# Performance work log

Measured on AMD Instinct MI355X. Metric: run time of the kernel, lower is better.

The kernel has to match this reference:

```python
import jax, jax.numpy as jnp
import numpy as np

HIDDEN = 1024
HEADS = 16
HEAD = HIDDEN // HEADS


def setup_inputs() -> dict:
    key = jax.random.key(0)
    k1, k2, k3, k4, k5, k6 = jax.random.split(key, 6)
    B, S = 2, 2048
    x = jax.random.normal(k1, (B, S, HIDDEN), dtype=jnp.float32)
    mask = jax.random.randint(k2, (B, S), 0, 2, dtype=jnp.int32)
    # torch nn.Linear params: W [out,in], b [out]
    s = 1.0 / np.sqrt(HIDDEN)
    qkv_w = jax.random.uniform(k3, (3 * HIDDEN, HIDDEN), jnp.float32, -s, s)
    qkv_b = jax.random.uniform(k4, (3 * HIDDEN,), jnp.float32, -s, s)
    out_w = jax.random.uniform(k5, (HIDDEN, HIDDEN), jnp.float32, -s, s)
    out_b = jax.random.uniform(k6, (HIDDEN,), jnp.float32, -s, s)
    return {"x": x, "mask": mask, "qkv_w": qkv_w, "qkv_b": qkv_b,
            "out_w": out_w, "out_b": out_b}


def reference(x, mask, qkv_w, qkv_b, out_w, out_b):
    B, S, H = x.shape
    scale = HEAD ** -0.5
    qkv = x @ qkv_w.T + qkv_b                      # [B,S,3H]
    qkv = qkv.reshape(B, S, 3, HEADS, HEAD)
    qkv = jnp.transpose(qkv, (2, 0, 3, 1, 4))      # [3,B,h,S,d]
    q, k, v = qkv[0], qkv[1], qkv[2]
    scores = jnp.einsum('bhqd,bhkd->bhqk', q, k) * scale
    # key-padding mask [B,S] -> [B,1,1,S]
    scores = jnp.where(mask[:, None, None, :] == 0, -1e9, scores)
    attn = jax.nn.softmax(scores, axis=-1)
    # dropout is identity in eval mode
    ctx = jnp.einsum('bhqk,bhkd->bhqd', attn, v)   # [B,h,S,d]
    ctx = jnp.transpose(ctx, (0, 2, 1, 3)).reshape(B, S, H)
    return ctx @ out_w.T + out_b
```

## Files before the change

kernel.cpp:

```cpp
#include <hip/hip_runtime.h>
#include <hip/hip_bf16.h>

#define S_LEN 2048
#define NH    16
#define HD    64
#define HID   1024
#define BATCH 2
#define STK   72

typedef __bf16 bf16x8 __attribute__((ext_vector_type(8)));
typedef float  f32x4  __attribute__((ext_vector_type(4)));

__device__ __forceinline__ unsigned int pk2(float lo, float hi) {
    union { __hip_bfloat162 h; unsigned int u; } c;
    c.h = __float22bfloat162_rn(make_float2(lo, hi));
    return c.u;
}
__device__ __forceinline__ uint4 pk8(float4 a, float4 b) {
    uint4 o;
    o.x = pk2(a.x, a.y); o.y = pk2(a.z, a.w);
    o.z = pk2(b.x, b.y); o.w = pk2(b.z, b.w);
    return o;
}
__device__ __forceinline__ float exp2_hw(float x) {
    float r; asm("v_exp_f32 %0, %1" : "=v"(r) : "v"(x)); return r;
}
__device__ __forceinline__ void gll16(const unsigned short* g, unsigned short* l) {
    __builtin_amdgcn_global_load_lds(
        (const __attribute__((address_space(1))) void*)g,
        (__attribute__((address_space(3))) void*)l, 16, 0, 0);
}

__global__ __launch_bounds__(256)
void fill_constf(float* __restrict__ out, long n, float v) {
    long i = (long)blockIdx.x * 256 + threadIdx.x;
    const long stride = (long)gridDim.x * 256;
    for (; i < n; i += stride) out[i] = v;
}

__global__ __launch_bounds__(256)
void cvt_bf16(const float* __restrict__ src, unsigned short* __restrict__ dst, long n8) {
    long t = (long)blockIdx.x * 256 + threadIdx.x;
    const long stride = (long)gridDim.x * 256;
    for (; t < n8; t += stride) {
        const float4 a = *(const float4*)(src + t * 8);
        const float4 b = *(const float4*)(src + t * 8 + 4);
        *(uint4*)(dst + t * 8) = pk8(a, b);
    }
}
__global__ __launch_bounds__(256)
void cvt2_bf16(const float* __restrict__ s0, unsigned short* __restrict__ d0, long n0,
               const float* __restrict__ s1, unsigned short* __restrict__ d1, long n1) {
    long t = (long)blockIdx.x * 256 + threadIdx.x;
    const long stride = (long)gridDim.x * 256;
    for (; t < n0 + n1; t += stride) {
        const float* s; unsigned short* d; long i;
        if (t < n0) { s = s0; d = d0; i = t; } else { s = s1; d = d1; i = t - n0; }
        const float4 a = *(const float4*)(s + i * 8);
        const float4 b = *(const float4*)(s + i * 8 + 4);
        *(uint4*)(d + i * 8) = pk8(a, b);
    }
}

__global__ __launch_bounds__(256)
void gemm_bf16(const unsigned short* __restrict__ A,
               const unsigned short* __restrict__ W,
               const float* __restrict__ bias,
               unsigned short* __restrict__ o0,
               unsigned short* __restrict__ o1,
               unsigned short* __restrict__ o2,
               float* __restrict__ of,
               int mode)
{
    __shared__ __align__(16) unsigned short lA[3][128 * 32];
    __shared__ __align__(16) unsigned short lB[3][128 * 32];
    const int tid  = threadIdx.x;
    const int lane = tid & 63, wv = tid >> 6;
    const int quad = lane >> 4, l16 = lane & 15;
    const int wm = (wv & 1) * 64, wn = (wv >> 1) * 64;

    const int nwg = gridDim.x * gridDim.y;
    const int bid = blockIdx.y * gridDim.x + blockIdx.x;
    const int xcd = bid & 7, boff = bid >> 3;
    const int qd = nwg >> 3, rm = nwg & 7;
    const int swz = (xcd < rm ? xcd * (qd + 1) : rm * (qd + 1) + (xcd - rm) * qd) + boff;
    const int m0 = (swz / gridDim.x) * 128, n0 = (swz % gridDim.x) * 128;

    f32x4 acc[4][4] = {};

    const int srow0 = wv * 32 + (lane >> 2);
    const int srow1 = srow0 + 16;
    const int csrc  = ((lane & 3) ^ ((lane >> 3) & 3)) * 8;
    const unsigned short* pa0 = A + (long)(m0 + srow0) * HID + csrc;
    const unsigned short* pa1 = A + (long)(m0 + srow1) * HID + csrc;
    const unsigned short* pb0 = W + (long)(n0 + srow0) * HID + csrc;
    const unsigned short* pb1 = W + (long)(n0 + srow1) * HID + csrc;

    const int cq8 = (quad ^ ((l16 >> 1) & 3)) * 8;

#define STAGE_G(bufi, koff)                                        \
    do {                                                           \
        gll16(pa0 + (koff), &lA[bufi][(wv * 2 + 0) * 512]);        \
        gll16(pa1 + (koff), &lA[bufi][(wv * 2 + 1) * 512]);        \
        gll16(pb0 + (koff), &lB[bufi][(wv * 2 + 0) * 512]);        \
        gll16(pb1 + (koff), &lB[bufi][(wv * 2 + 1) * 512]);        \
    } while (0)

    STAGE_G(0, 0);
    STAGE_G(1, 32);

    int cur = 0;
    for (int k0 = 0; k0 < HID; k0 += 32) {
        if (k0 + 32 < HID) { asm volatile("s_waitcnt vmcnt(4)" ::: "memory"); }
        else               { asm volatile("s_waitcnt vmcnt(0)" ::: "memory"); }
        __builtin_amdgcn_s_barrier();
        asm volatile("" ::: "memory");

        if (k0 + 64 < HID) {
            const int nxt = cur ? cur - 1 : 2;
            STAGE_G(nxt, k0 + 64);
        }

        bf16x8 af[4], bfr[4];
#pragma unroll
        for (int mt = 0; mt < 4; mt++)
            af[mt] = *(const bf16x8*)&lA[cur][(wm + mt * 16 + l16) * 32 + cq8];
#pragma unroll
        for (int nt = 0; nt < 4; nt++)
            bfr[nt] = *(const bf16x8*)&lB[cur][(wn + nt * 16 + l16) * 32 + cq8];
#pragma unroll
        for (int mt = 0; mt < 4; mt++)
#pragma unroll
            for (int nt = 0; nt < 4; nt++)
                acc[mt][nt] = __builtin_amdgcn_mfma_f32_16x16x32_bf16(
                    af[mt], bfr[nt], acc[mt][nt], 0, 0, 0);

        cur = (cur < 2) ? cur + 1 : 0;
    }
#undef STAGE_G

    if (mode == 0) {
#pragma unroll
        for (int nt = 0; nt < 4; nt++) {
            const int n = n0 + wn + nt * 16 + l16;
            const float bv = bias[n];
            const int part = n >> 10, f = n & 1023, h = f >> 6, d = f & 63;
#pragma unroll
            for (int mt = 0; mt < 4; mt++) {
                const int mbase = m0 + wm + mt * 16 + quad * 4;
                const int b = mbase >> 11, s0 = mbase & 2047;
                const int bh = b * NH + h;
                if (part == 2) {
                    uint2 o;
                    o.x = pk2(acc[mt][nt][0] + bv, acc[mt][nt][1] + bv);
                    o.y = pk2(acc[mt][nt][2] + bv, acc[mt][nt][3] + bv);
                    *(uint2*)&o2[((long)bh * HD + d) * S_LEN + s0] = o;
                } else {
                    unsigned short* dst = (part == 0) ? o0 : o1;
#pragma unroll
                    for (int r = 0; r < 4; r++) {
                        union { __hip_bfloat16 h; unsigned short u; } cv;
                        cv.h = __float2bfloat16(acc[mt][nt][r] + bv);
                        dst[((long)bh * S_LEN + s0 + r) * HD + d] = cv.u;
                    }
                }
            }
        }
    } else {
#pragma unroll
        for (int nt = 0; nt < 4; nt++) {
            const int n = n0 + wn + nt * 16 + l16;
            const float bv = bias[n];
#pragma unroll
            for (int mt = 0; mt < 4; mt++) {
                const int mbase = m0 + wm + mt * 16 + quad * 4;
#pragma unroll
                for (int r = 0; r < 4; r++)
                    of[(long)(mbase + r) * HID + n] = acc[mt][nt][r] + bv;
            }
        }
    }
}

__global__ __launch_bounds__(512)
void attn(const unsigned short* __restrict__ q,
          const unsigned short* __restrict__ k,
          const unsigned short* __restrict__ vt_g,
          const int* __restrict__ mask,
          unsigned short* __restrict__ ctx)
{
    __shared__ __align__(16) unsigned short kt[64 * STK];
    __shared__ __align__(16) unsigned short vt[64 * STK];
    __shared__ __align__(16) __bf16 pt[8][16 * 72];
    __shared__ float mkv[64];

    const int tid  = threadIdx.x;
    const int lane = tid & 63, wv = tid >> 6;
    const int quad = lane >> 4, l16 = lane & 15;
    const int qt = blockIdx.x, h = blockIdx.y, b = blockIdx.z;
    const int bh = b * NH + h;
    const float SC = 0.18033688f;

    const int sq = qt * 128 + wv * 16 + l16;
    bf16x8 qf0 = *(const bf16x8*)&q[((long)bh * S_LEN + sq) * HD + quad * 8];
    bf16x8 qf1 = *(const bf16x8*)&q[((long)bh * S_LEN + sq) * HD + 32 + quad * 8];

    float mrun = -1e30f, lrun = 0.f;
    f32x4 Of[4] = {};

    const int sr = tid >> 3, sc8 = (tid & 7) * 8;
    const unsigned short* kg = k    + ((long)bh * S_LEN + sr) * HD + sc8;
    const unsigned short* vg = vt_g + ((long)bh * HD + sr) * S_LEN + sc8;
    __bf16* ptw = pt[wv];

    uint4 rk = *(const uint4*)(kg);
    uint4 rv = *(const uint4*)(vg);
    float rm = 0.f;
    if (tid < 64) rm = (mask[b * S_LEN + tid] == 0) ? -1e9f : 0.f;

    for (int k0 = 0; k0 < S_LEN; k0 += 64) {
        *(uint4*)&kt[sr * STK + sc8] = rk;
        *(uint4*)&vt[sr * STK + sc8] = rv;
        if (tid < 64) mkv[tid] = rm;
        if (k0 + 64 < S_LEN) {
            rk = *(const uint4*)(kg + (long)(k0 + 64) * HD);
            rv = *(const uint4*)(vg + (k0 + 64));
            if (tid < 64) rm = (mask[b * S_LEN + k0 + 64 + tid] == 0) ? -1e9f : 0.f;
        }
        __syncthreads();

        float st[4][4];
#pragma unroll
        for (int nt = 0; nt < 4; nt++) {
            bf16x8 k0f = *(const bf16x8*)&kt[(nt * 16 + l16) * STK + quad * 8];
            bf16x8 k1f = *(const bf16x8*)&kt[(nt * 16 + l16) * STK + 32 + quad * 8];
            f32x4 s = {};
            s = __builtin_amdgcn_mfma_f32_16x16x32_bf16(k0f, qf0, s, 0, 0, 0);
            s = __builtin_amdgcn_mfma_f32_16x16x32_bf16(k1f, qf1, s, 0, 0, 0);
            const float4 mv = *(const float4*)&mkv[nt * 16 + quad * 4];
#pragma unroll
            for (int r = 0; r < 4; r++) st[nt][r] = fmaf(s[r], SC, (&mv.x)[r]);
        }

        float mx = st[0][0];
#pragma unroll
        for (int nt = 0; nt < 4; nt++)
#pragma unroll
            for (int r = 0; r < 4; r++) mx = fmaxf(mx, st[nt][r]);
        mx = fmaxf(mx, __shfl_xor(mx, 16, 64));
        mx = fmaxf(mx, __shfl_xor(mx, 32, 64));
        const float mn = fmaxf(mrun, mx);
        const float alpha = exp2_hw(mrun - mn);
        float pr[4][4];
#pragma unroll
        for (int nt = 0; nt < 4; nt++)
#pragma unroll
            for (int r = 0; r < 4; r++) pr[nt][r] = exp2_hw(st[nt][r] - mn);
        float rs = 0.f;
#pragma unroll
        for (int nt = 0; nt < 4; nt++)
#pragma unroll
            for (int r = 0; r < 4; r++) rs += pr[nt][r];
        rs += __shfl_xor(rs, 16, 64);
        rs += __shfl_xor(rs, 32, 64);
        lrun = lrun * alpha + rs;
        mrun = mn;

#pragma unroll
        for (int nt = 0; nt < 4; nt++) {
            const unsigned long long lo = pk2(pr[nt][0], pr[nt][1]);
            const unsigned long long hi = pk2(pr[nt][2], pr[nt][3]);
            *(unsigned long long*)&ptw[l16 * 72 + nt * 16 + quad * 4] = lo | (hi << 32);
        }
        asm volatile("" ::: "memory");

#pragma unroll
        for (int nt = 0; nt < 4; nt++) Of[nt] *= alpha;

#pragma unroll
        for (int ks = 0; ks < 2; ks++) {
            bf16x8 bp = *(const bf16x8*)&ptw[l16 * 72 + ks * 32 + quad * 8];
#pragma unroll
            for (int nt = 0; nt < 4; nt++) {
                bf16x8 av = *(const bf16x8*)&vt[(nt * 16 + l16) * STK + ks * 32 + quad * 8];
                Of[nt] = __builtin_amdgcn_mfma_f32_16x16x32_bf16(av, bp, Of[nt], 0, 0, 0);
            }
        }
        __syncthreads();
    }

    const float inv = 1.f / lrun;
#pragma unroll
    for (int nt = 0; nt < 4; nt++) {
        uint2 o;
        o.x = pk2(Of[nt][0] * inv, Of[nt][1] * inv);
        o.y = pk2(Of[nt][2] * inv, Of[nt][3] * inv);
        *(uint2*)&ctx[((long)b * S_LEN + sq) * HID + h * HD + nt * 16 + quad * 4] = o;
    }
}

extern "C" void kernel_launch(void* const* d_in, const int* in_sizes, int n_in,
                              void* d_out, int out_size, void* d_ws, size_t ws_size,
                              hipStream_t stream) {
    float* outp = (float*)d_out;

    const float* x = nullptr; const int* mask = nullptr;
    const float* qkv_w = nullptr; const float* qkv_b = nullptr;
    const float* out_w = nullptr; const float* out_b = nullptr;
    for (int i = 0; i < n_in; i++) {
        switch (in_sizes[i]) {
            case 4194304: x     = (const float*)d_in[i]; break;
            case 4096:    mask  = (const int*)d_in[i];   break;
            case 3145728: qkv_w = (const float*)d_in[i]; break;
            case 3072:    qkv_b = (const float*)d_in[i]; break;
            case 1048576: out_w = (const float*)d_in[i]; break;
            case 1024:    out_b = (const float*)d_in[i]; break;
            default: break;
        }
    }
    if (!x || !mask || !qkv_w || !qkv_b || !out_w || !out_b) {
        fill_constf<<<256, 256, 0, stream>>>(outp, (long)out_size, 1000.0f);
        return;
    }

    const size_t per = (size_t)BATCH * NH * S_LEN * HD;
    const size_t nx  = (size_t)BATCH * S_LEN * HID;
    const size_t nqw = (size_t)3 * HID * HID;
    const size_t now = (size_t)HID * HID;
    if (ws_size < 4 * per * sizeof(unsigned short)) {
        fill_constf<<<256, 256, 0, stream>>>(outp, (long)out_size, 2000.0f);
        return;
    }

    unsigned short* wsq = (unsigned short*)d_ws;
    unsigned short* wsk = wsq + per;
    unsigned short* wsv = wsk + per;
    unsigned short* wsc = wsv + per;
    unsigned short* xb  = wsc;
    unsigned short* qwb = (unsigned short*)d_out;
    unsigned short* owb = wsq;

    cvt2_bf16<<<1024, 256, 0, stream>>>(x, xb, (long)(nx / 8), qkv_w, qwb, (long)(nqw / 8));
    gemm_bf16<<<dim3(3 * HID / 128, BATCH * S_LEN / 128), 256, 0, stream>>>(
        xb, qwb, qkv_b, wsq, wsk, wsv, nullptr, 0);
    attn<<<dim3(S_LEN / 128, NH, BATCH), 512, 0, stream>>>(wsq, wsk, wsv, mask, wsc);
    cvt_bf16<<<512, 256, 0, stream>>>(out_w, owb, (long)(now / 8));
    gemm_bf16<<<dim3(HID / 128, BATCH * S_LEN / 128), 256, 0, stream>>>(
        wsc, owb, out_b, nullptr, nullptr, nullptr, outp, 1);
}
```

Before: 236.7 us.

## Double-buffer K/V tiles, fold softmax scale into Q, lazily rescale online softmax

The attention kernel now double-buffers the K, V and mask tiles in shared memory, so each iteration has a single barrier and the next tile is stored while the current one is computed. The softmax scale (with log2e) is folded into Q during the projection epilogue, and the mask is fed in as the MFMA accumulator init, which removes the per-score FMA. The running max is only updated when the new max exceeds the old one by more than 8, which skips most of the alpha rescaling of O and l. In exchange shared memory use roughly doubles for K/V, which may reduce occupancy, and the lazy max lets exponents reach 2^8 before rescaling.

Result: faster. 231.4 us (-2.2%).

```diff
diff --git a/kernel.cpp b/kernel.cpp
--- a/kernel.cpp
+++ b/kernel.cpp
@@ -7,6 +7,7 @@
 #define HID   1024
 #define BATCH 2
 #define STK   72
+#define SCQ   0.18033688f
 
 typedef __bf16 bf16x8 __attribute__((ext_vector_type(8)));
 typedef float  f32x4  __attribute__((ext_vector_type(4)));
@@ -157,10 +158,11 @@
                     *(uint2*)&o2[((long)bh * HD + d) * S_LEN + s0] = o;
                 } else {
                     unsigned short* dst = (part == 0) ? o0 : o1;
+                    const float qsc = (part == 0) ? SCQ : 1.0f;
 #pragma unroll
                     for (int r = 0; r < 4; r++) {
                         union { __hip_bfloat16 h; unsigned short u; } cv;
-                        cv.h = __float2bfloat16(acc[mt][nt][r] + bv);
+                        cv.h = __float2bfloat16((acc[mt][nt][r] + bv) * qsc);
                         dst[((long)bh * S_LEN + s0 + r) * HD + d] = cv.u;
                     }
                 }
@@ -189,17 +191,16 @@
           const int* __restrict__ mask,
           unsigned short* __restrict__ ctx)
 {
-    __shared__ __align__(16) unsigned short kt[64 * STK];
-    __shared__ __align__(16) unsigned short vt[64 * STK];
+    __shared__ __align__(16) unsigned short kt[2][64 * STK];
+    __shared__ __align__(16) unsigned short vt[2][64 * STK];
     __shared__ __align__(16) __bf16 pt[8][16 * 72];
-    __shared__ float mkv[64];
+    __shared__ float mkv[2][64];
 
     const int tid  = threadIdx.x;
     const int lane = tid & 63, wv = tid >> 6;
     const int quad = lane >> 4, l16 = lane & 15;
     const int qt = blockIdx.x, h = blockIdx.y, b = blockIdx.z;
     const int bh = b * NH + h;
-    const float SC = 0.18033688f;
 
     const int sq = qt * 128 + wv * 16 + l16;
     bf16x8 qf0 = *(const bf16x8*)&q[((long)bh * S_LEN + sq) * HD + quad * 8];
@@ -217,54 +218,72 @@
     uint4 rv = *(const uint4*)(vg);
     float rm = 0.f;
     if (tid < 64) rm = (mask[b * S_LEN + tid] == 0) ? -1e9f : 0.f;
+    *(uint4*)&kt[0][sr * STK + sc8] = rk;
+    *(uint4*)&vt[0][sr * STK + sc8] = rv;
+    if (tid < 64) mkv[0][tid] = rm;
+    rk = *(const uint4*)(kg + (long)64 * HD);
+    rv = *(const uint4*)(vg + 64);
+    if (tid < 64) rm = (mask[b * S_LEN + 64 + tid] == 0) ? -1e9f : 0.f;
+    asm volatile("s_waitcnt lgkmcnt(0)" ::: "memory");
+    __builtin_amdgcn_s_barrier();
+    asm volatile("" ::: "memory");
 
     for (int k0 = 0; k0 < S_LEN; k0 += 64) {
-        *(uint4*)&kt[sr * STK + sc8] = rk;
-        *(uint4*)&vt[sr * STK + sc8] = rv;
-        if (tid < 64) mkv[tid] = rm;
+        const int cur = (k0 >> 6) & 1;
         if (k0 + 64 < S_LEN) {
-            rk = *(const uint4*)(kg + (long)(k0 + 64) * HD);
-            rv = *(const uint4*)(vg + (k0 + 64));
-            if (tid < 64) rm = (mask[b * S_LEN + k0 + 64 + tid] == 0) ? -1e9f : 0.f;
-        }
-        __syncthreads();
+            *(uint4*)&kt[cur ^ 1][sr * STK + sc8] = rk;
+            *(uint4*)&vt[cur ^ 1][sr * STK + sc8] = rv;
+            if (tid < 64) mkv[cur ^ 1][tid] = rm;
+            if (k0 + 128 < S_LEN) {
+                rk = *(const uint4*)(kg + (long)(k0 + 128) * HD);
+                rv = *(const uint4*)(vg + (k0 + 128));
+                if (tid < 64) rm = (mask[b * S_LEN + k0 + 128 + tid] == 0) ? -1e9f : 0.f;
+            }
+        }
 
         float st[4][4];
 #pragma unroll
         for (int nt = 0; nt < 4; nt++) {
-            bf16x8 k0f = *(const bf16x8*)&kt[(nt * 16 + l16) * STK + quad * 8];
-            bf16x8 k1f = *(const bf16x8*)&kt[(nt * 16 + l16) * STK + 32 + quad * 8];
-            f32x4 s = {};
+            bf16x8 k0f = *(const bf16x8*)&kt[cur][(nt * 16 + l16) * STK + quad * 8];
+            bf16x8 k1f = *(const bf16x8*)&kt[cur][(nt * 16 + l16) * STK + 32 + quad * 8];
+            const float4 mv = *(const float4*)&mkv[cur][nt * 16 + quad * 4];
+            f32x4 s = {mv.x, mv.y, mv.z, mv.w};
             s = __builtin_amdgcn_mfma_f32_16x16x32_bf16(k0f, qf0, s, 0, 0, 0);
             s = __builtin_amdgcn_mfma_f32_16x16x32_bf16(k1f, qf1, s, 0, 0, 0);
-            const float4 mv = *(const float4*)&mkv[nt * 16 + quad * 4];
-#pragma unroll
-            for (int r = 0; r < 4; r++) st[nt][r] = fmaf(s[r], SC, (&mv.x)[r]);
-        }
-
-        float mx = st[0][0];
+#pragma unroll
+            for (int r = 0; r < 4; r++) st[nt][r] = s[r];
+        }
+
+        float mxa[4];
 #pragma unroll
         for (int nt = 0; nt < 4; nt++)
-#pragma unroll
-            for (int r = 0; r < 4; r++) mx = fmaxf(mx, st[nt][r]);
+            mxa[nt] = fmaxf(fmaxf(st[nt][0], st[nt][1]), fmaxf(st[nt][2], st[nt][3]));
+        float mx = fmaxf(fmaxf(mxa[0], mxa[1]), fmaxf(mxa[2], mxa[3]));
         mx = fmaxf(mx, __shfl_xor(mx, 16, 64));
         mx = fmaxf(mx, __shfl_xor(mx, 32, 64));
-        const float mn = fmaxf(mrun, mx);
-        const float alpha = exp2_hw(mrun - mn);
+
+        if (!__all(mx <= mrun + 8.f)) {
+            const float mn = fmaxf(mrun, mx);
+            const float alpha = exp2_hw(mrun - mn);
+#pragma unroll
+            for (int nt = 0; nt < 4; nt++) Of[nt] *= alpha;
+            lrun *= alpha;
+            mrun = mn;
+        }
+
         float pr[4][4];
 #pragma unroll
         for (int nt = 0; nt < 4; nt++)
 #pragma unroll
-            for (int r = 0; r < 4; r++) pr[nt][r] = exp2_hw(st[nt][r] - mn);
-        float rs = 0.f;
+            for (int r = 0; r < 4; r++) pr[nt][r] = exp2_hw(st[nt][r] - mrun);
+        float rsa[4];
 #pragma unroll
         for (int nt = 0; nt < 4; nt++)
-#pragma unroll
-            for (int r = 0; r < 4; r++) rs += pr[nt][r];
+            rsa[nt] = (pr[nt][0] + pr[nt][1]) + (pr[nt][2] + pr[nt][3]);
+        float rs = (rsa[0] + rsa[1]) + (rsa[2] + rsa[3]);
         rs += __shfl_xor(rs, 16, 64);
         rs += __shfl_xor(rs, 32, 64);
-        lrun = lrun * alpha + rs;
-        mrun = mn;
+        lrun += rs;
 
 #pragma unroll
         for (int nt = 0; nt < 4; nt++) {
@@ -275,18 +294,18 @@
         asm volatile("" ::: "memory");
 
 #pragma unroll
-        for (int nt = 0; nt < 4; nt++) Of[nt] *= alpha;
-
-#pragma unroll
         for (int ks = 0; ks < 2; ks++) {
             bf16x8 bp = *(const bf16x8*)&ptw[l16 * 72 + ks * 32 + quad * 8];
 #pragma unroll
             for (int nt = 0; nt < 4; nt++) {
-                bf16x8 av = *(const bf16x8*)&vt[(nt * 16 + l16) * STK + ks * 32 + quad * 8];
+                bf16x8 av = *(const bf16x8*)&vt[cur][(nt * 16 + l16) * STK + ks * 32 + quad * 8];
                 Of[nt] = __builtin_amdgcn_mfma_f32_16x16x32_bf16(av, bp, Of[nt], 0, 0, 0);
             }
         }
-        __syncthreads();
+
+        asm volatile("s_waitcnt lgkmcnt(0)" ::: "memory");
+        __builtin_amdgcn_s_barrier();
+        asm volatile("" ::: "memory");
     }
 
     const float inv = 1.f / lrun;
```
